# Kernel tuning notes

Measured on AMD Instinct MI355X. Metric: run time of the kernel, lower is better.

The kernel has to match this reference:

```python
import jax, jax.numpy as jnp
import numpy as np

NUM_HEADS = 16
NEG_INF = -1e30


def setup_inputs() -> dict:
    key = jax.random.key(0)
    k1, k2, k3 = jax.random.split(key, 3)
    B, S, D = 2, 2048, 1024
    x = jax.random.normal(k1, (B, S, D), dtype=jnp.float32)
    # torch Linear(D, 3D, bias=False) stored here already transposed: y = x @ w_qkv
    w_qkv = jax.random.normal(k2, (D, 3 * D), dtype=jnp.float32) * 0.02
    w_out = jax.random.normal(k3, (D, D), dtype=jnp.float32) * 0.02
    return {"x": x, "w_qkv": w_qkv, "w_out": w_out}


def reference(x, w_qkv, w_out):
    B, S, D = x.shape
    H = NUM_HEADS
    dh = D // H
    qkv = x @ w_qkv                      # [B, S, 3D]
    q, k, v = jnp.split(qkv, 3, axis=-1)

    def to_heads(t):
        return t.reshape(B, S, H, dh).transpose(0, 2, 1, 3)  # [B, H, S, dh]

    q, k, v = to_heads(q), to_heads(k), to_heads(v)
    scale = jnp.asarray(dh, x.dtype) ** -0.5
    scores = jnp.einsum('bhqd,bhkd->bhqk', q, k) * scale     # [B, H, S, S]
    causal = jnp.tril(jnp.ones((S, S), dtype=bool))
    scores = jnp.where(causal, scores, NEG_INF)
    attn = jax.nn.softmax(scores, axis=-1)
    out = jnp.einsum('bhqk,bhkd->bhqd', attn, v)             # [B, H, S, dh]
    out = out.transpose(0, 2, 1, 3).reshape(B, S, D)
    return out @ w_out
```

## Files before the change

### kernel.cpp

```cpp
#include <hip/hip_runtime.h>

typedef unsigned short u16;
typedef unsigned int u32;

typedef __bf16 bf16x8 __attribute__((ext_vector_type(8)));
typedef _Float16 f16x8 __attribute__((ext_vector_type(8)));
typedef float f32x4 __attribute__((ext_vector_type(4)));

typedef __attribute__((address_space(1))) u32 as1_u32;
typedef __attribute__((address_space(3))) u32 as3_u32;

#define EKF 0.18033688011112042f

__device__ __forceinline__ u16 f2bf(float x) {
  u32 u = __float_as_uint(x);
  u = u + 0x7fffu + ((u >> 16) & 1u);
  return (u16)(u >> 16);
}
__device__ __forceinline__ u32 pack2(float a, float b) {
  return (u32)f2bf(a) | ((u32)f2bf(b) << 16);
}
__device__ __forceinline__ u32 pkf16(float a, float b) {
  return __builtin_bit_cast(u32, __builtin_amdgcn_cvt_pkrtz(a, b));
}
__device__ __forceinline__ u16 f2h(float a) {
  return (u16)(pkf16(a, a) & 0xffffu);
}
__device__ __forceinline__ void gld_lds16(const u16* g, const u16* l) {
  __builtin_amdgcn_global_load_lds((const as1_u32*)g, (as3_u32*)l, 16, 0, 0);
}

__global__ __launch_bounds__(256) void prepass_kernel(const float* __restrict__ x,
                                                      const float* __restrict__ w_qkv,
                                                      const float* __restrict__ w_out,
                                                      u16* __restrict__ xb,
                                                      u16* __restrict__ wqkvT,
                                                      u16* __restrict__ woutT) {
  __shared__ float tile[64][65];
  int bid = blockIdx.x;
  int t = threadIdx.x;
  if (bid < 4096) {
    int i = bid * 256 + t;
    float4 v = ((const float4*)x)[i];
    uint2 r;
    r.x = pack2(v.x, v.y);
    r.y = pack2(v.z, v.w);
    ((uint2*)xb)[i] = r;
    return;
  }
  const float* W;
  u16* WT;
  int K, N, bx, by;
  if (bid < 4096 + 768) {
    int b2 = bid - 4096;
    W = w_qkv; WT = wqkvT; K = 1024; N = 3072; bx = b2 & 15; by = b2 >> 4;
  } else {
    int b2 = bid - 4864;
    W = w_out; WT = woutT; K = 1024; N = 1024; bx = b2 & 15; by = b2 >> 4;
  }
  int k0 = bx * 64, n0 = by * 64;
  int r = t >> 4, c4 = (t & 15) * 4;
#pragma unroll
  for (int i = 0; i < 4; ++i) {
    int row = r + i * 16;
    float4 v = *(const float4*)&W[(size_t)(k0 + row) * N + n0 + c4];
    tile[row][c4 + 0] = v.x; tile[row][c4 + 1] = v.y;
    tile[row][c4 + 2] = v.z; tile[row][c4 + 3] = v.w;
  }
  __syncthreads();
#pragma unroll
  for (int i = 0; i < 4; ++i) {
    int n = r + i * 16;
    uint2 o;
    o.x = pack2(tile[c4 + 0][n], tile[c4 + 1][n]);
    o.y = pack2(tile[c4 + 2][n], tile[c4 + 3][n]);
    *(uint2*)&WT[(size_t)(n0 + n) * K + k0 + c4] = o;
  }
}

__global__ __launch_bounds__(512, 2) void gemm_qkv256_kernel(const u16* __restrict__ A,
                                                             const u16* __restrict__ BT,
                                                             u16* __restrict__ QK,
                                                             u16* __restrict__ VT) {
  __shared__ __attribute__((aligned(16))) u16 smem[65536];
  const int tid = threadIdx.x;
  const int wave = tid >> 6;
  const int lane = tid & 63;
  const int lr = lane & 15;
  const int kg = lane >> 4;
  const int l7 = lr & 7;
  const int wr = wave >> 2;
  const int wc = wave & 3;

  int b = blockIdx.x;
  int sw = (b & 7) * 24 + (b >> 3);
  const int bn = (sw % 12) * 256;
  const int bm = (sw / 12) * 256;

  const int srow = tid >> 3;
  const int scg = ((tid & 7) ^ (srow & 7)) * 8;
  const u16* pa = A + (size_t)(bm + srow) * 1024 + scg;
  const u16* pb = BT + (size_t)(bn + srow) * 1024 + scg;
  const u32 lw = (u32)wave * 512;

  f32x4 acc[8][4];
#pragma unroll
  for (int i = 0; i < 8; ++i)
#pragma unroll
    for (int j = 0; j < 4; ++j) {
      f32x4 z = {0.f, 0.f, 0.f, 0.f};
      acc[i][j] = z;
    }

  {
    u16* dA = (u16*)smem;
    u16* dB = (u16*)smem + 16384;
#pragma unroll
    for (int i = 0; i < 4; ++i) gld_lds16(pa + (size_t)(i * 64) * 1024, dA + lw + i * 4096);
#pragma unroll
    for (int i = 0; i < 4; ++i) gld_lds16(pb + (size_t)(i * 64) * 1024, dB + lw + i * 4096);
  }

  for (int t = 0; t < 16; ++t) {
    __syncthreads();
    const u16* bA = smem + (t & 1) * 32768;
    const u16* bB = bA + 16384;
    if (t + 1 < 16) {
      u16* dA = (u16*)smem + ((t + 1) & 1) * 32768;
      u16* dB = dA + 16384;
      const int k1 = (t + 1) * 64;
#pragma unroll
      for (int i = 0; i < 4; ++i) gld_lds16(pa + (size_t)(i * 64) * 1024 + k1, dA + lw + i * 4096);
#pragma unroll
      for (int i = 0; i < 4; ++i) gld_lds16(pb + (size_t)(i * 64) * 1024 + k1, dB + lw + i * 4096);
    }
    bf16x8 bfr[2][4];
#pragma unroll
    for (int kh = 0; kh < 2; ++kh)
#pragma unroll
      for (int ni = 0; ni < 4; ++ni)
        bfr[kh][ni] = *(const bf16x8*)(bB + (wc * 64 + ni * 16 + lr) * 64 +
                                       (((kh * 4 + kg) ^ l7) * 8));
#pragma unroll
    for (int ph = 0; ph < 4; ++ph) {
      const int mh = ph >> 1, kh = ph & 1;
      bf16x8 af[4];
#pragma unroll
      for (int mi = 0; mi < 4; ++mi)
        af[mi] = *(const bf16x8*)(bA + (wr * 128 + mh * 64 + mi * 16 + lr) * 64 +
                                  (((kh * 4 + kg) ^ l7) * 8));
      __builtin_amdgcn_s_barrier();
      __builtin_amdgcn_s_setprio(1);
#pragma unroll
      for (int mi = 0; mi < 4; ++mi)
#pragma unroll
        for (int ni = 0; ni < 4; ++ni)
          acc[mh * 4 + mi][ni] = __builtin_amdgcn_mfma_f32_16x16x32_bf16(
              bfr[kh][ni], af[mi], acc[mh * 4 + mi][ni], 0, 0, 0);
      __builtin_amdgcn_s_setprio(0);
      __builtin_amdgcn_s_barrier();
    }
  }

  __syncthreads();
  if (bn >= 2048) {
#pragma unroll
    for (int mi = 0; mi < 8; ++mi)
#pragma unroll
      for (int ni = 0; ni < 4; ++ni) {
        int r = bm + wr * 128 + mi * 16 + lr;
        int c = bn + wc * 64 + ni * 16 + kg * 4 - 2048;
        int bh2 = (r >> 11) * 16 + (c >> 6);
        int j = r & 2047;
        u16* vrow = VT + ((size_t)bh2 * 64 + (c & 63)) * 2048 + j;
        f32x4 a = acc[mi][ni];
#pragma unroll
        for (int rr = 0; rr < 4; ++rr) vrow[(size_t)rr * 2048] = f2h(a[rr]);
      }
  } else {
    float scale = (bn < 1024) ? EKF : 1.0f;
#pragma unroll
    for (int mi = 0; mi < 8; ++mi)
#pragma unroll
      for (int ni = 0; ni < 4; ++ni) {
        int row = wr * 128 + mi * 16 + lr;
        u32 off = (u32)row * 256 + wc * 64 + (((ni * 4 + kg) ^ (lr & 6)) * 4);
        f32x4 a = acc[mi][ni];
        *(uint2*)((u16*)smem + off) =
            make_uint2(pack2(a[0] * scale, a[1] * scale), pack2(a[2] * scale, a[3] * scale));
      }
    __syncthreads();
#pragma unroll
    for (int i = 0; i < 16; ++i) {
      int row = i * 16 + (tid >> 5);
      int lc = tid & 31;
      int blk = lc >> 3, cc = lc & 7;
      uint4 v = *(const uint4*)((const u16*)smem + (u32)row * 256 + blk * 64 +
                                (((2 * cc) ^ (row & 6)) * 4));
      *(uint4*)(QK + (size_t)(bm + row) * 2048 + bn + blk * 64 + cc * 8) = v;
    }
  }
}

template <int OUT_MODE, int BN>
__global__ __launch_bounds__(256) void gemm_bt_kernel(const u16* __restrict__ A,
                                                      const u16* __restrict__ BT,
                                                      void* __restrict__ Cv,
                                                      u16* __restrict__ VT,
                                                      int M, int N, int K) {
  const int NF = (BN == 128) ? 4 : 2;
  __shared__ __attribute__((aligned(16))) u16 sA[128 * 64];
  __shared__ __attribute__((aligned(16))) u16 sB[BN * 64];
  const int tid = threadIdx.x;
  const int wave = tid >> 6;
  const int lane = tid & 63;
  const int bm = blockIdx.y * 128;
  const int bn = blockIdx.x * BN;
  const int wm = (wave >> 1) * 64;
  const int wn = (wave & 1) * (BN / 2);
  const int lr = lane & 15;
  const int kg = lane >> 4;
  const int lr7 = lr & 7;

  const int sr = tid >> 3;
  const int sc = tid & 7;
  const int scg = (sc ^ (sr & 7)) * 8;
  const u16* pa = A + (size_t)(bm + sr) * K + scg;
  const u16* pb = BT + (size_t)(bn + sr) * K + scg;
  const u16* la = sA + wave * 512;
  const u16* lb = sB + wave * 512;

  f32x4 acc[4][NF];
#pragma unroll
  for (int i = 0; i < 4; i++)
#pragma unroll
    for (int j = 0; j < NF; j++) {
      f32x4 z = {0.f, 0.f, 0.f, 0.f};
      acc[i][j] = z;
    }

  for (int k0 = 0; k0 < K; k0 += 64) {
    __syncthreads();
#pragma unroll
    for (int i = 0; i < 4; ++i)
      gld_lds16(pa + (size_t)(i * 32) * K + k0, la + i * 2048);
#pragma unroll
    for (int i = 0; i < NF; ++i)
      gld_lds16(pb + (size_t)(i * 32) * K + k0, lb + i * 2048);
    __syncthreads();
#pragma unroll
    for (int kk = 0; kk < 2; ++kk) {
      bf16x8 af[4], bfr[NF];
      const int ch = ((kk * 4 + kg) ^ lr7) * 8;
#pragma unroll
      for (int mi = 0; mi < 4; mi++)
        af[mi] = *(const bf16x8*)(sA + (wm + mi * 16 + lr) * 64 + ch);
#pragma unroll
      for (int ni = 0; ni < NF; ni++)
        bfr[ni] = *(const bf16x8*)(sB + (wn + ni * 16 + lr) * 64 + ch);
#pragma unroll
      for (int mi = 0; mi < 4; mi++)
#pragma unroll
        for (int ni = 0; ni < NF; ni++)
          acc[mi][ni] = __builtin_amdgcn_mfma_f32_16x16x32_bf16(bfr[ni], af[mi], acc[mi][ni], 0, 0, 0);
    }
  }

  if (OUT_MODE == 0) {
    float* buf = (float*)sA;
    float* outp = (float*)Cv;
#pragma unroll
    for (int hc = 0; hc < 2; ++hc) {
      __syncthreads();
      if ((wave & 1) == hc) {
#pragma unroll
        for (int mi = 0; mi < 4; mi++)
#pragma unroll
          for (int ni = 0; ni < NF; ni++) {
            int row = wm + mi * 16 + lr;
            int cp = ((ni * 4 + kg) ^ lr7) * 4;
            *(f32x4*)(buf + row * 32 + cp) = acc[mi][ni];
          }
      }
      __syncthreads();
#pragma unroll
      for (int i = 0; i < 4; ++i) {
        int row = i * 32 + (tid >> 3);
        int lc = tid & 7;
        float4 v = *(const float4*)(buf + row * 32 + ((lc ^ (row & 7)) * 4));
        *(float4*)(outp + (size_t)(bm + row) * N + bn + hc * 32 + lc * 4) = v;
      }
    }
  } else if (bn >= 2048) {
#pragma unroll
    for (int mi = 0; mi < 4; mi++)
#pragma unroll
      for (int ni = 0; ni < NF; ni++) {
        int r = bm + wm + mi * 16 + lr;
        int cc = bn + wn + ni * 16 + kg * 4 - 2048;
        int bh2 = (r >> 11) * 16 + (cc >> 6);
        int j = r & 2047;
        u16* vrow = VT + ((size_t)bh2 * 64 + (cc & 63)) * 2048 + j;
        f32x4 a = acc[mi][ni];
#pragma unroll
        for (int rr = 0; rr < 4; rr++)
          vrow[(size_t)rr * 2048] = f2h(a[rr]);
      }
  } else {
    float scale = (bn < 1024) ? EKF : 1.0f;
    u16* buf = sA;
    u16* qkp = (u16*)Cv;
#pragma unroll
    for (int hc = 0; hc < 2; ++hc) {
      __syncthreads();
      if ((wave & 1) == hc) {
#pragma unroll
        for (int mi = 0; mi < 4; mi++)
#pragma unroll
          for (int ni = 0; ni < NF; ni++) {
            int row = wm + mi * 16 + lr;
            int sp = ((ni * 4 + kg) ^ (lr & 6)) * 4;
            f32x4 a = acc[mi][ni];
            *(uint2*)(buf + row * 64 + sp) =
                make_uint2(pack2(a[0] * scale, a[1] * scale),
                           pack2(a[2] * scale, a[3] * scale));
          }
      }
      __syncthreads();
#pragma unroll
      for (int i = 0; i < 4; ++i) {
        int row = i * 32 + (tid >> 3);
        int lc = tid & 7;
        uint4 v = *(const uint4*)(buf + row * 64 + (((2 * lc) ^ (row & 6)) * 4));
        *(uint4*)(qkp + (size_t)(bm + row) * 2048 + bn + hc * 64 + lc * 8) = v;
      }
    }
  }
}

__global__ __launch_bounds__(256, 4) void attn_mfma_kernel(const u16* __restrict__ qk,
                                                           const u16* __restrict__ vt,
                                                           u16* __restrict__ out) {
  __shared__ __attribute__((aligned(16))) u16 sK[2][64 * 64];
  __shared__ __attribute__((aligned(16))) u16 sV[2][64 * 64];
  __shared__ __attribute__((aligned(16))) u16 sP[4][16 * 64];

  const int tid = threadIdx.x;
  const int wave = tid >> 6;
  const int lane = tid & 63;
  const int lr = lane & 15;
  const int kg = lane >> 4;
  const int l7 = lr & 7;

  int idx = blockIdx.x;
  int qi = 31 - (idx >> 5);
  int bh = idx & 31;
  int b = bh >> 4, h = bh & 15;
  int q0 = qi * 64;

  const u16* qbase = qk + (size_t)b * 2048 * 2048 + h * 64;
  const u16* kbase = qbase + 1024;
  const u16* vbase = vt + (size_t)bh * 64 * 2048;
  u16* obase = out + (size_t)b * 2048 * 1024 + h * 64;

  const int sra = wave * 16 + (lane >> 3);
  const int srb = sra + 8;
  const int sc = lane & 7;
  const u32 koffA = (u32)sra * 2048 + (u32)((sc ^ (sra & 7)) * 8);
  const u32 koffB = (u32)srb * 2048 + (u32)((sc ^ (srb & 7)) * 8);
  const u32 ldsA = (wave * 2 + 0) * 512;
  const u32 ldsB = (wave * 2 + 1) * 512;

  const int qcol = q0 + wave * 16 + lr;
  bf16x8 qf0, qf1;
  {
    const u16* qrow = qbase + (size_t)qcol * 2048;
    qf0 = *(const bf16x8*)(qrow + kg * 8);
    qf1 = *(const bf16x8*)(qrow + 32 + kg * 8);
  }

  const u32 ka0 = (u32)(lr * 64 + ((kg ^ l7) * 8));
  const u32 ka1 = (u32)(lr * 64 + (((4 + kg) ^ l7) * 8));
  u16* const sPw = sP[wave];
  const u32 pr0 = (u32)(lr * 64 + (((kg * 2) ^ (l7 << 1)) * 4));
  const u32 pr1 = (u32)(lr * 64 + (((8 + kg * 2) ^ (l7 << 1)) * 4));

  f32x4 oacc[4];
#pragma unroll
  for (int i = 0; i < 4; ++i) {
    f32x4 z = {0.f, 0.f, 0.f, 0.f};
    oacc[i] = z;
  }
  float lsum = 0.f;

  const int nrounds = qi + 1;
  gld_lds16(kbase + koffA, sK[0] + ldsA);
  gld_lds16(kbase + koffB, sK[0] + ldsB);
  gld_lds16(vbase + koffA, sV[0] + ldsA);
  gld_lds16(vbase + koffB, sV[0] + ldsB);
  __syncthreads();

  for (int t = 0; t < nrounds; ++t) {
    if (t + 1 < nrounds) {
      int j1 = (t + 1) * 64;
      u16* dK = sK[(t + 1) & 1];
      u16* dV = sV[(t + 1) & 1];
      gld_lds16(kbase + (size_t)j1 * 2048 + koffA, dK + ldsA);
      gld_lds16(kbase + (size_t)j1 * 2048 + koffB, dK + ldsB);
      gld_lds16(vbase + j1 + koffA, dV + ldsA);
      gld_lds16(vbase + j1 + koffB, dV + ldsB);
    }
    const u16* sKb = sK[t & 1];
    const u16* sVb = sV[t & 1];
    const bool diag = (t == qi);

#pragma unroll
    for (int jt = 0; jt < 4; ++jt) {
      u16* pw = sPw + lr * 64 + (((jt * 4 + kg) ^ (l7 << 1)) * 4);
      if (!diag || jt <= wave) {
        bf16x8 kf0 = *(const bf16x8*)(sKb + jt * 1024 + ka0);
        bf16x8 kf1 = *(const bf16x8*)(sKb + jt * 1024 + ka1);
        f32x4 c = {0.f, 0.f, 0.f, 0.f};
        c = __builtin_amdgcn_mfma_f32_16x16x32_bf16(kf0, qf0, c, 0, 0, 0);
        c = __builtin_amdgcn_mfma_f32_16x16x32_bf16(kf1, qf1, c, 0, 0, 0);
        float p0 = exp2f(c[0]);
        float p1 = exp2f(c[1]);
        float p2 = exp2f(c[2]);
        float p3 = exp2f(c[3]);
        if (diag && jt == wave) {
          int jr = kg * 4;
          p0 = (jr + 0 <= lr) ? p0 : 0.f;
          p1 = (jr + 1 <= lr) ? p1 : 0.f;
          p2 = (jr + 2 <= lr) ? p2 : 0.f;
          p3 = (jr + 3 <= lr) ? p3 : 0.f;
        }
        lsum += (p0 + p1) + (p2 + p3);
        *(uint2*)pw = make_uint2(pkf16(p0, p1), pkf16(p2, p3));
      } else {
        *(uint2*)pw = make_uint2(0u, 0u);
      }
    }

    asm volatile("" ::: "memory");

    f16x8 pf0 = *(const f16x8*)(sPw + pr0);
    f16x8 pf1 = *(const f16x8*)(sPw + pr1);
#pragma unroll
    for (int dt = 0; dt < 4; ++dt) {
      f16x8 vf0 = *(const f16x8*)(sVb + dt * 1024 + ka0);
      f16x8 vf1 = *(const f16x8*)(sVb + dt * 1024 + ka1);
      oacc[dt] = __builtin_amdgcn_mfma_f32_16x16x32_f16(vf0, pf0, oacc[dt], 0, 0, 0);
      oacc[dt] = __builtin_amdgcn_mfma_f32_16x16x32_f16(vf1, pf1, oacc[dt], 0, 0, 0);
    }
    __syncthreads();
  }

  lsum += __shfl_xor(lsum, 16);
  lsum += __shfl_xor(lsum, 32);
  float inv = 1.0f / lsum;

  u16* orow = obase + (size_t)qcol * 1024;
#pragma unroll
  for (int dt = 0; dt < 4; ++dt) {
    uint2 o2 = make_uint2(pack2(oacc[dt][0] * inv, oacc[dt][1] * inv),
                          pack2(oacc[dt][2] * inv, oacc[dt][3] * inv));
    *(uint2*)(orow + dt * 16 + kg * 4) = o2;
  }
}

extern "C" void kernel_launch(void* const* d_in, const int* in_sizes, int n_in,
                              void* d_out, int out_size, void* d_ws, size_t ws_size,
                              hipStream_t stream) {
  const float* x = (const float*)d_in[0];
  const float* w_qkv = (const float*)d_in[1];
  const float* w_out = (const float*)d_in[2];
  float* out = (float*)d_out;

  char* ws = (char*)d_ws;
  u16* xb    = (u16*)(ws);
  u16* wqkvT = (u16*)(ws + (8u << 20));
  u16* woutT = (u16*)(ws + (14u << 20));
  u16* qkb   = (u16*)(ws + (16u << 20));
  u16* vtb   = (u16*)(ws + (32u << 20));
  u16* attn  = (u16*)(ws + (40u << 20));

  prepass_kernel<<<5120, 256, 0, stream>>>(x, w_qkv, w_out, xb, wqkvT, woutT);

  gemm_qkv256_kernel<<<192, 512, 0, stream>>>(xb, wqkvT, qkb, vtb);

  attn_mfma_kernel<<<1024, 256, 0, stream>>>(qkb, vtb, attn);

  gemm_bt_kernel<0, 64><<<dim3(1024 / 64, 4096 / 128), 256, 0, stream>>>(
      attn, woutT, (void*)out, nullptr, 4096, 1024, 1024);
}
```

Baseline: 169.0 us.

## Rewrite attention with 32x32 MFMA, 128-row query tiles and register-resident P

```diff
diff --git a/kernel.cpp b/kernel.cpp
--- a/kernel.cpp
+++ b/kernel.cpp
@@ -6,6 +6,8 @@
 typedef __bf16 bf16x8 __attribute__((ext_vector_type(8)));
 typedef _Float16 f16x8 __attribute__((ext_vector_type(8)));
 typedef float f32x4 __attribute__((ext_vector_type(4)));
+typedef float f32x16 __attribute__((ext_vector_type(16)));
+typedef u32 u32x4 __attribute__((ext_vector_type(4)));
 
 typedef __attribute__((address_space(1))) u32 as1_u32;
 typedef __attribute__((address_space(3))) u32 as3_u32;
@@ -338,25 +340,23 @@
   }
 }
 
-__global__ __launch_bounds__(256, 4) void attn_mfma_kernel(const u16* __restrict__ qk,
-                                                           const u16* __restrict__ vt,
-                                                           u16* __restrict__ out) {
+__global__ __launch_bounds__(256, 2) void attn_mfma32_kernel(const u16* __restrict__ qk,
+                                                             const u16* __restrict__ vt,
+                                                             u16* __restrict__ out) {
   __shared__ __attribute__((aligned(16))) u16 sK[2][64 * 64];
   __shared__ __attribute__((aligned(16))) u16 sV[2][64 * 64];
-  __shared__ __attribute__((aligned(16))) u16 sP[4][16 * 64];
 
   const int tid = threadIdx.x;
   const int wave = tid >> 6;
   const int lane = tid & 63;
-  const int lr = lane & 15;
-  const int kg = lane >> 4;
-  const int l7 = lr & 7;
+  const int l31 = lane & 31;
+  const int hi = lane >> 5;
 
   int idx = blockIdx.x;
-  int qi = 31 - (idx >> 5);
   int bh = idx & 31;
+  int qi = (idx < 256) ? (15 - (idx >> 5)) : ((idx - 256) >> 5);
   int b = bh >> 4, h = bh & 15;
-  int q0 = qi * 64;
+  int q0 = qi * 128;
 
   const u16* qbase = qk + (size_t)b * 2048 * 2048 + h * 64;
   const u16* kbase = qbase + 1024;
@@ -371,29 +371,23 @@
   const u32 ldsA = (wave * 2 + 0) * 512;
   const u32 ldsB = (wave * 2 + 1) * 512;
 
-  const int qcol = q0 + wave * 16 + lr;
-  bf16x8 qf0, qf1;
+  const int qcol = q0 + wave * 32 + l31;
+  bf16x8 qf[4];
   {
     const u16* qrow = qbase + (size_t)qcol * 2048;
-    qf0 = *(const bf16x8*)(qrow + kg * 8);
-    qf1 = *(const bf16x8*)(qrow + 32 + kg * 8);
-  }
-
-  const u32 ka0 = (u32)(lr * 64 + ((kg ^ l7) * 8));
-  const u32 ka1 = (u32)(lr * 64 + (((4 + kg) ^ l7) * 8));
-  u16* const sPw = sP[wave];
-  const u32 pr0 = (u32)(lr * 64 + (((kg * 2) ^ (l7 << 1)) * 4));
-  const u32 pr1 = (u32)(lr * 64 + (((8 + kg * 2) ^ (l7 << 1)) * 4));
-
-  f32x4 oacc[4];
-#pragma unroll
-  for (int i = 0; i < 4; ++i) {
-    f32x4 z = {0.f, 0.f, 0.f, 0.f};
-    oacc[i] = z;
-  }
+#pragma unroll
+    for (int s = 0; s < 4; ++s) qf[s] = *(const bf16x8*)(qrow + s * 16 + hi * 8);
+  }
+
+  f32x16 oacc[2];
+#pragma unroll
+  for (int i = 0; i < 16; ++i) { oacc[0][i] = 0.f; oacc[1][i] = 0.f; }
   float lsum = 0.f;
 
-  const int nrounds = qi + 1;
+  const int nrounds = 2 * qi + 2;
+  const int tfull = (q0 + 32 * wave) >> 6;
+  const int tlast = (q0 + 32 * wave + 31) >> 6;
+
   gld_lds16(kbase + koffA, sK[0] + ldsA);
   gld_lds16(kbase + koffB, sK[0] + ldsB);
   gld_lds16(vbase + koffA, sV[0] + ldsA);
@@ -412,60 +406,73 @@
     }
     const u16* sKb = sK[t & 1];
     const u16* sVb = sV[t & 1];
-    const bool diag = (t == qi);
-
-#pragma unroll
-    for (int jt = 0; jt < 4; ++jt) {
-      u16* pw = sPw + lr * 64 + (((jt * 4 + kg) ^ (l7 << 1)) * 4);
-      if (!diag || jt <= wave) {
-        bf16x8 kf0 = *(const bf16x8*)(sKb + jt * 1024 + ka0);
-        bf16x8 kf1 = *(const bf16x8*)(sKb + jt * 1024 + ka1);
-        f32x4 c = {0.f, 0.f, 0.f, 0.f};
-        c = __builtin_amdgcn_mfma_f32_16x16x32_bf16(kf0, qf0, c, 0, 0, 0);
-        c = __builtin_amdgcn_mfma_f32_16x16x32_bf16(kf1, qf1, c, 0, 0, 0);
-        float p0 = exp2f(c[0]);
-        float p1 = exp2f(c[1]);
-        float p2 = exp2f(c[2]);
-        float p3 = exp2f(c[3]);
-        if (diag && jt == wave) {
-          int jr = kg * 4;
-          p0 = (jr + 0 <= lr) ? p0 : 0.f;
-          p1 = (jr + 1 <= lr) ? p1 : 0.f;
-          p2 = (jr + 2 <= lr) ? p2 : 0.f;
-          p3 = (jr + 3 <= lr) ? p3 : 0.f;
+
+    if (t <= tlast) {
+      f16x8 pa[4];
+      const int qrel = qcol - t * 64;
+      const bool masked = (t >= tfull);
+#pragma unroll
+      for (int jh = 0; jh < 2; ++jh) {
+        f32x16 c;
+#pragma unroll
+        for (int i = 0; i < 16; ++i) c[i] = 0.f;
+#pragma unroll
+        for (int s = 0; s < 4; ++s) {
+          const u32 row = (u32)(jh * 32 + l31);
+          bf16x8 kf = *(const bf16x8*)(sKb + row * 64 + (((2 * s + hi) ^ (row & 7)) * 8));
+          c = __builtin_amdgcn_mfma_f32_32x32x16_bf16(kf, qf[s], c, 0, 0, 0);
         }
-        lsum += (p0 + p1) + (p2 + p3);
-        *(uint2*)pw = make_uint2(pkf16(p0, p1), pkf16(p2, p3));
-      } else {
-        *(uint2*)pw = make_uint2(0u, 0u);
-      }
-    }
-
-    asm volatile("" ::: "memory");
-
-    f16x8 pf0 = *(const f16x8*)(sPw + pr0);
-    f16x8 pf1 = *(const f16x8*)(sPw + pr1);
-#pragma unroll
-    for (int dt = 0; dt < 4; ++dt) {
-      f16x8 vf0 = *(const f16x8*)(sVb + dt * 1024 + ka0);
-      f16x8 vf1 = *(const f16x8*)(sVb + dt * 1024 + ka1);
-      oacc[dt] = __builtin_amdgcn_mfma_f32_16x16x32_f16(vf0, pf0, oacc[dt], 0, 0, 0);
-      oacc[dt] = __builtin_amdgcn_mfma_f32_16x16x32_f16(vf1, pf1, oacc[dt], 0, 0, 0);
+        float p[16];
+#pragma unroll
+        for (int r = 0; r < 16; ++r) {
+          int joff = jh * 32 + (r & 3) + 8 * (r >> 2) + 4 * hi;
+          float e = exp2f(c[r]);
+          p[r] = (!masked || (joff <= qrel)) ? e : 0.f;
+        }
+        float s0 = (p[0] + p[1]) + (p[2] + p[3]);
+        float s1 = (p[4] + p[5]) + (p[6] + p[7]);
+        float s2 = (p[8] + p[9]) + (p[10] + p[11]);
+        float s3 = (p[12] + p[13]) + (p[14] + p[15]);
+        lsum += (s0 + s1) + (s2 + s3);
+        u32 c01 = pkf16(p[0], p[1]),  c23 = pkf16(p[2], p[3]);
+        u32 c45 = pkf16(p[4], p[5]),  c67 = pkf16(p[6], p[7]);
+        u32 c89 = pkf16(p[8], p[9]),  cab = pkf16(p[10], p[11]);
+        u32 ccd = pkf16(p[12], p[13]), cef = pkf16(p[14], p[15]);
+        asm volatile("v_permlane32_swap_b32 %0, %1" : "+v"(c01), "+v"(c45));
+        asm volatile("v_permlane32_swap_b32 %0, %1" : "+v"(c23), "+v"(c67));
+        asm volatile("v_permlane32_swap_b32 %0, %1" : "+v"(c89), "+v"(ccd));
+        asm volatile("v_permlane32_swap_b32 %0, %1" : "+v"(cab), "+v"(cef));
+        u32x4 w0 = {c01, c23, c45, c67};
+        u32x4 w1 = {c89, cab, ccd, cef};
+        pa[2 * jh + 0] = __builtin_bit_cast(f16x8, w0);
+        pa[2 * jh + 1] = __builtin_bit_cast(f16x8, w1);
+      }
+      __builtin_amdgcn_s_setprio(1);
+#pragma unroll
+      for (int dh = 0; dh < 2; ++dh)
+#pragma unroll
+        for (int s = 0; s < 4; ++s) {
+          const u32 row = (u32)(dh * 32 + l31);
+          f16x8 vf = *(const f16x8*)(sVb + row * 64 + (((2 * s + hi) ^ (row & 7)) * 8));
+          oacc[dh] = __builtin_amdgcn_mfma_f32_32x32x16_f16(vf, pa[s], oacc[dh], 0, 0, 0);
+        }
+      __builtin_amdgcn_s_setprio(0);
     }
     __syncthreads();
   }
 
-  lsum += __shfl_xor(lsum, 16);
   lsum += __shfl_xor(lsum, 32);
   float inv = 1.0f / lsum;
 
   u16* orow = obase + (size_t)qcol * 1024;
 #pragma unroll
-  for (int dt = 0; dt < 4; ++dt) {
-    uint2 o2 = make_uint2(pack2(oacc[dt][0] * inv, oacc[dt][1] * inv),
-                          pack2(oacc[dt][2] * inv, oacc[dt][3] * inv));
-    *(uint2*)(orow + dt * 16 + kg * 4) = o2;
-  }
+  for (int dh = 0; dh < 2; ++dh)
+#pragma unroll
+    for (int g = 0; g < 4; ++g) {
+      uint2 o2 = make_uint2(pack2(oacc[dh][4 * g + 0] * inv, oacc[dh][4 * g + 1] * inv),
+                            pack2(oacc[dh][4 * g + 2] * inv, oacc[dh][4 * g + 3] * inv));
+      *(uint2*)(orow + dh * 32 + g * 8 + hi * 4) = o2;
+    }
 }
 
 extern "C" void kernel_launch(void* const* d_in, const int* in_sizes, int n_in,
@@ -488,7 +495,7 @@
 
   gemm_qkv256_kernel<<<192, 512, 0, stream>>>(xb, wqkvT, qkb, vtb);
 
-  attn_mfma_kernel<<<1024, 256, 0, stream>>>(qkb, vtb, attn);
+  attn_mfma32_kernel<<<512, 256, 0, stream>>>(qkb, vtb, attn);
 
   gemm_bt_kernel<0, 64><<<dim3(1024 / 64, 4096 / 128), 256, 0, stream>>>(
       attn, woutT, (void*)out, nullptr, 4096, 1024, 1024);
```

Result: slower. 188.0 us (+11.2%).

## Double-buffer output projection GEMM with XCD-aware tiling and MFMA priority hints

Applied to the files above, without the earlier changes.

```diff
diff --git a/kernel.cpp b/kernel.cpp
--- a/kernel.cpp
+++ b/kernel.cpp
@@ -202,138 +202,102 @@
   }
 }
 
-template <int OUT_MODE, int BN>
-__global__ __launch_bounds__(256) void gemm_bt_kernel(const u16* __restrict__ A,
-                                                      const u16* __restrict__ BT,
-                                                      void* __restrict__ Cv,
-                                                      u16* __restrict__ VT,
-                                                      int M, int N, int K) {
-  const int NF = (BN == 128) ? 4 : 2;
-  __shared__ __attribute__((aligned(16))) u16 sA[128 * 64];
-  __shared__ __attribute__((aligned(16))) u16 sB[BN * 64];
+__global__ __launch_bounds__(256, 2) void gemm_out_kernel(const u16* __restrict__ A,
+                                                          const u16* __restrict__ BT,
+                                                          float* __restrict__ C) {
+  __shared__ __attribute__((aligned(16))) u16 smem[2][12288];
   const int tid = threadIdx.x;
   const int wave = tid >> 6;
   const int lane = tid & 63;
-  const int bm = blockIdx.y * 128;
-  const int bn = blockIdx.x * BN;
-  const int wm = (wave >> 1) * 64;
-  const int wn = (wave & 1) * (BN / 2);
   const int lr = lane & 15;
   const int kg = lane >> 4;
   const int lr7 = lr & 7;
+  const int wm = (wave >> 1) * 32;
+  const int wn = (wave & 1) * 64;
+
+  const int b = blockIdx.x;
+  const int xcd = b & 7, loc = b >> 3;
+  const int bm = (xcd * 8 + (loc >> 3)) * 64;
+  const int bn = (loc & 7) * 128;
 
   const int sr = tid >> 3;
-  const int sc = tid & 7;
-  const int scg = (sc ^ (sr & 7)) * 8;
-  const u16* pa = A + (size_t)(bm + sr) * K + scg;
-  const u16* pb = BT + (size_t)(bn + sr) * K + scg;
-  const u16* la = sA + wave * 512;
-  const u16* lb = sB + wave * 512;
-
-  f32x4 acc[4][NF];
-#pragma unroll
-  for (int i = 0; i < 4; i++)
-#pragma unroll
-    for (int j = 0; j < NF; j++) {
+  const int scg = ((tid & 7) ^ (sr & 7)) * 8;
+  const u16* pa = A + (size_t)(bm + sr) * 1024 + scg;
+  const u16* pb = BT + (size_t)(bn + sr) * 1024 + scg;
+  const u32 lw = (u32)wave * 512;
+
+  f32x4 acc[2][4];
+#pragma unroll
+  for (int i = 0; i < 2; ++i)
+#pragma unroll
+    for (int j = 0; j < 4; ++j) {
       f32x4 z = {0.f, 0.f, 0.f, 0.f};
       acc[i][j] = z;
     }
 
-  for (int k0 = 0; k0 < K; k0 += 64) {
-    __syncthreads();
-#pragma unroll
-    for (int i = 0; i < 4; ++i)
-      gld_lds16(pa + (size_t)(i * 32) * K + k0, la + i * 2048);
-#pragma unroll
-    for (int i = 0; i < NF; ++i)
-      gld_lds16(pb + (size_t)(i * 32) * K + k0, lb + i * 2048);
-    __syncthreads();
+  {
+    u16* dA = smem[0];
+    u16* dB = smem[0] + 4096;
+#pragma unroll
+    for (int i = 0; i < 2; ++i) gld_lds16(pa + (size_t)(i * 32) * 1024, dA + lw + i * 2048);
+#pragma unroll
+    for (int i = 0; i < 4; ++i) gld_lds16(pb + (size_t)(i * 32) * 1024, dB + lw + i * 2048);
+  }
+
+  for (int t = 0; t < 16; ++t) {
+    __syncthreads();
+    const u16* bA = smem[t & 1];
+    const u16* bB = bA + 4096;
+    if (t + 1 < 16) {
+      u16* dA = smem[(t + 1) & 1];
+      u16* dB = dA + 4096;
+      const int k1 = (t + 1) * 64;
+#pragma unroll
+      for (int i = 0; i < 2; ++i) gld_lds16(pa + (size_t)(i * 32) * 1024 + k1, dA + lw + i * 2048);
+#pragma unroll
+      for (int i = 0; i < 4; ++i) gld_lds16(pb + (size_t)(i * 32) * 1024 + k1, dB + lw + i * 2048);
+    }
 #pragma unroll
     for (int kk = 0; kk < 2; ++kk) {
-      bf16x8 af[4], bfr[NF];
       const int ch = ((kk * 4 + kg) ^ lr7) * 8;
-#pragma unroll
-      for (int mi = 0; mi < 4; mi++)
-        af[mi] = *(const bf16x8*)(sA + (wm + mi * 16 + lr) * 64 + ch);
-#pragma unroll
-      for (int ni = 0; ni < NF; ni++)
-        bfr[ni] = *(const bf16x8*)(sB + (wn + ni * 16 + lr) * 64 + ch);
-#pragma unroll
-      for (int mi = 0; mi < 4; mi++)
-#pragma unroll
-        for (int ni = 0; ni < NF; ni++)
+      bf16x8 af[2], bfr[4];
+#pragma unroll
+      for (int mi = 0; mi < 2; ++mi)
+        af[mi] = *(const bf16x8*)(bA + (wm + mi * 16 + lr) * 64 + ch);
+#pragma unroll
+      for (int ni = 0; ni < 4; ++ni)
+        bfr[ni] = *(const bf16x8*)(bB + (wn + ni * 16 + lr) * 64 + ch);
+      __builtin_amdgcn_s_setprio(1);
+#pragma unroll
+      for (int mi = 0; mi < 2; ++mi)
+#pragma unroll
+        for (int ni = 0; ni < 4; ++ni)
           acc[mi][ni] = __builtin_amdgcn_mfma_f32_16x16x32_bf16(bfr[ni], af[mi], acc[mi][ni], 0, 0, 0);
-    }
-  }
-
-  if (OUT_MODE == 0) {
-    float* buf = (float*)sA;
-    float* outp = (float*)Cv;
-#pragma unroll
-    for (int hc = 0; hc < 2; ++hc) {
-      __syncthreads();
-      if ((wave & 1) == hc) {
-#pragma unroll
-        for (int mi = 0; mi < 4; mi++)
-#pragma unroll
-          for (int ni = 0; ni < NF; ni++) {
-            int row = wm + mi * 16 + lr;
-            int cp = ((ni * 4 + kg) ^ lr7) * 4;
-            *(f32x4*)(buf + row * 32 + cp) = acc[mi][ni];
-          }
-      }
-      __syncthreads();
-#pragma unroll
-      for (int i = 0; i < 4; ++i) {
-        int row = i * 32 + (tid >> 3);
-        int lc = tid & 7;
-        float4 v = *(const float4*)(buf + row * 32 + ((lc ^ (row & 7)) * 4));
-        *(float4*)(outp + (size_t)(bm + row) * N + bn + hc * 32 + lc * 4) = v;
-      }
-    }
-  } else if (bn >= 2048) {
-#pragma unroll
-    for (int mi = 0; mi < 4; mi++)
-#pragma unroll
-      for (int ni = 0; ni < NF; ni++) {
-        int r = bm + wm + mi * 16 + lr;
-        int cc = bn + wn + ni * 16 + kg * 4 - 2048;
-        int bh2 = (r >> 11) * 16 + (cc >> 6);
-        int j = r & 2047;
-        u16* vrow = VT + ((size_t)bh2 * 64 + (cc & 63)) * 2048 + j;
-        f32x4 a = acc[mi][ni];
-#pragma unroll
-        for (int rr = 0; rr < 4; rr++)
-          vrow[(size_t)rr * 2048] = f2h(a[rr]);
-      }
-  } else {
-    float scale = (bn < 1024) ? EKF : 1.0f;
-    u16* buf = sA;
-    u16* qkp = (u16*)Cv;
-#pragma unroll
-    for (int hc = 0; hc < 2; ++hc) {
-      __syncthreads();
-      if ((wave & 1) == hc) {
-#pragma unroll
-        for (int mi = 0; mi < 4; mi++)
-#pragma unroll
-          for (int ni = 0; ni < NF; ni++) {
-            int row = wm + mi * 16 + lr;
-            int sp = ((ni * 4 + kg) ^ (lr & 6)) * 4;
-            f32x4 a = acc[mi][ni];
-            *(uint2*)(buf + row * 64 + sp) =
-                make_uint2(pack2(a[0] * scale, a[1] * scale),
-                           pack2(a[2] * scale, a[3] * scale));
-          }
-      }
-      __syncthreads();
-#pragma unroll
-      for (int i = 0; i < 4; ++i) {
-        int row = i * 32 + (tid >> 3);
-        int lc = tid & 7;
-        uint4 v = *(const uint4*)(buf + row * 64 + (((2 * lc) ^ (row & 6)) * 4));
-        *(uint4*)(qkp + (size_t)(bm + row) * 2048 + bn + hc * 64 + lc * 8) = v;
-      }
+      __builtin_amdgcn_s_setprio(0);
+    }
+  }
+
+  float* buf = (float*)smem;
+#pragma unroll
+  for (int hc = 0; hc < 2; ++hc) {
+    __syncthreads();
+    if ((wave & 1) == hc) {
+#pragma unroll
+      for (int mi = 0; mi < 2; ++mi)
+#pragma unroll
+        for (int ni = 0; ni < 4; ++ni) {
+          int row = wm + mi * 16 + lr;
+          int cp = ((ni * 4 + kg) ^ lr) * 4;
+          *(f32x4*)(buf + row * 64 + cp) = acc[mi][ni];
+        }
+    }
+    __syncthreads();
+#pragma unroll
+    for (int i = 0; i < 4; ++i) {
+      int row = i * 16 + (tid >> 4);
+      int lc = tid & 15;
+      float4 v = *(const float4*)(buf + row * 64 + ((lc ^ (row & 15)) * 4));
+      *(float4*)(C + (size_t)(bm + row) * 1024 + bn + hc * 64 + lc * 4) = v;
     }
   }
 }
@@ -445,6 +409,7 @@
 
     f16x8 pf0 = *(const f16x8*)(sPw + pr0);
     f16x8 pf1 = *(const f16x8*)(sPw + pr1);
+    __builtin_amdgcn_s_setprio(1);
 #pragma unroll
     for (int dt = 0; dt < 4; ++dt) {
       f16x8 vf0 = *(const f16x8*)(sVb + dt * 1024 + ka0);
@@ -452,6 +417,7 @@
       oacc[dt] = __builtin_amdgcn_mfma_f32_16x16x32_f16(vf0, pf0, oacc[dt], 0, 0, 0);
       oacc[dt] = __builtin_amdgcn_mfma_f32_16x16x32_f16(vf1, pf1, oacc[dt], 0, 0, 0);
     }
+    __builtin_amdgcn_s_setprio(0);
     __syncthreads();
   }
 
@@ -490,6 +456,5 @@
 
   attn_mfma_kernel<<<1024, 256, 0, stream>>>(qkb, vtb, attn);
 
-  gemm_bt_kernel<0, 64><<<dim3(1024 / 64, 4096 / 128), 256, 0, stream>>>(
-      attn, woutT, (void*)out, nullptr, 4096, 1024, 1024);
-}
+  gemm_out_kernel<<<512, 256, 0, stream>>>(attn, woutT, out);
+}
```

After: 163.7 us. 1.03x faster.
